# Performance work log

Hardware: AMD Instinct MI355X
Metric: run time of the kernel (lower is better)

## Reference

```python
import jax, jax.numpy as jnp
import numpy as np

B, D, T, H, E = 4, 1024, 2048, 16, 64  # batch, dim, seq_len, n_heads, hidden_dim (H*E == D)


def setup_inputs() -> dict:
    key = jax.random.key(0)
    ks = jax.random.split(key, 6)
    x = jax.random.normal(ks[0], (B, D, T), dtype=jnp.float32)            # (b, e, t) layout
    Wp = jax.random.normal(ks[1], (H, E, D), dtype=jnp.float32) / np.sqrt(D)  # per-head proj weights
    bp = jax.random.normal(ks[2], (H, E), dtype=jnp.float32) * 0.01
    tw = jax.random.normal(ks[3], (H, T), dtype=jnp.float32) / np.sqrt(T)  # per-head Toeplitz kernel, tw[h,0]=diagonal
    Wo = jax.random.normal(ks[4], (D, D), dtype=jnp.float32) / np.sqrt(D)
    bo = jax.random.normal(ks[5], (D,), dtype=jnp.float32) * 0.01
    return {"x": x, "Wp": Wp, "bp": bp, "tw": tw, "Wo": Wo, "bo": bo}


def reference(x, Wp, bp, tw, Wo, bo):
    # x: (b, dim, t) -> (b, t, dim)
    xt = jnp.transpose(x, (0, 2, 1))
    # per-head projections: (b, h, e, t)
    proj = jnp.einsum('btd,hed->bhet', xt, Wp) + bp[None, :, :, None]
    # build per-head causal lower-triangular Toeplitz matrices: Tm[h, t, s] = tw[h, t-s] if s <= t else 0
    idx = jnp.arange(T)[:, None] - jnp.arange(T)[None, :]  # (t, s)
    Tm = jnp.where(idx >= 0, tw[:, jnp.clip(idx, 0)], 0.0)  # (h, t, s)
    # causal Toeplitz mixing along time per head
    mixed = jnp.einsum('hts,bhes->bhet', Tm, proj)          # (b, h, e, t)
    # concat heads on feature dim: (b, t, h*e) == (b, t, dim)
    cat = jnp.transpose(mixed, (0, 3, 1, 2)).reshape(B, T, H * E)
    out = cat @ Wo.T + bo                                   # out_proj: Linear(dim, dim)
    return jnp.transpose(out, (0, 2, 1))                    # back to (b, e, t)
```

## Files before the change

### kernel.cpp

```cpp
#include <hip/hip_runtime.h>
#include <cstdint>

#define NB 4
#define ND 1024
#define NT 2048
#define NH 16
#define NE 64
#define GLEN 2240
#define CAP 2312

typedef __bf16 bf16x8 __attribute__((ext_vector_type(8)));
typedef float f32x4 __attribute__((ext_vector_type(4)));
typedef unsigned short us8 __attribute__((ext_vector_type(8)));
typedef unsigned short us4 __attribute__((ext_vector_type(4)));

__device__ __forceinline__ unsigned short f2bf(float f) {
  unsigned u = __builtin_bit_cast(unsigned, f);
  return (unsigned short)((u + 0x7fffu + ((u >> 16) & 1u)) >> 16);
}

__device__ __forceinline__ void gload16(const void* g, void* l) {
  __builtin_amdgcn_global_load_lds(
      (const __attribute__((address_space(1))) void*)(uintptr_t)g,
      (__attribute__((address_space(3))) void*)(uintptr_t)l, 16, 0, 0);
}

__global__ void prep_kernel(const float* __restrict__ Wp, const float* __restrict__ Wo,
                            const float* __restrict__ tw,
                            unsigned short* __restrict__ WpB, unsigned short* __restrict__ WoB,
                            unsigned short* __restrict__ Gr8) {
  int idx = blockIdx.x * 256 + threadIdx.x;
  int stride = gridDim.x * 256;
  const int n4 = ND * ND / 4;
  for (int i = idx; i < n4; i += stride) {
    float4 v = ((const float4*)Wp)[i];
    us4 o = {f2bf(v.x), f2bf(v.y), f2bf(v.z), f2bf(v.w)};
    ((us4*)WpB)[i] = o;
  }
  for (int i = idx; i < n4; i += stride) {
    float4 v = ((const float4*)Wo)[i];
    us4 o = {f2bf(v.x), f2bf(v.y), f2bf(v.z), f2bf(v.w)};
    ((us4*)WoB)[i] = o;
  }
  for (int i = idx; i < NH * 8 * GLEN; i += stride) {
    int h = i / (8 * GLEN);
    int rem = i - h * 8 * GLEN;
    int r = rem / GLEN;
    int c = rem - r * GLEN;
    int src = c + r;
    Gr8[i] = (src <= NT - 1) ? f2bf(tw[h * NT + (NT - 1) - src]) : (unsigned short)0;
  }
}

__global__ __launch_bounds__(256) void transpose_cast(const float* __restrict__ x,
                                                      unsigned short* __restrict__ xT) {
  __shared__ float tile[64][65];
  const int c = threadIdx.x & 15, r = threadIdx.x >> 4;
  const int t0 = blockIdx.x * 64, d0 = blockIdx.y * 64, b = blockIdx.z;
  const float* xb = x + (long)b * ND * NT;
#pragma unroll
  for (int k = 0; k < 4; ++k) {
    float4 v = *(const float4*)&xb[(long)(d0 + r + 16 * k) * NT + t0 + 4 * c];
    tile[r + 16 * k][4 * c + 0] = v.x;
    tile[r + 16 * k][4 * c + 1] = v.y;
    tile[r + 16 * k][4 * c + 2] = v.z;
    tile[r + 16 * k][4 * c + 3] = v.w;
  }
  __syncthreads();
  unsigned short* xTb = xT + (long)b * NT * ND;
#pragma unroll
  for (int k = 0; k < 4; ++k) {
    int t = r + 16 * k;
    us4 o = {f2bf(tile[4 * c + 0][t]), f2bf(tile[4 * c + 1][t]), f2bf(tile[4 * c + 2][t]),
             f2bf(tile[4 * c + 3][t])};
    *(us4*)&xTb[(long)(t0 + t) * ND + d0 + 4 * c] = o;
  }
}

template <bool OUT_BF16>
__global__ __launch_bounds__(512, 2) void gemm_bt(const unsigned short* __restrict__ A,
                                                  const unsigned short* __restrict__ Bt,
                                                  const float* __restrict__ bias,
                                                  void* __restrict__ Cb, long strideB,
                                                  long strideC) {
  const int N = 2048, K = 1024;
  __shared__ __align__(16) unsigned short As[3][128 * 64];
  __shared__ __align__(16) unsigned short Bs[3][256 * 64];
  const int tid = threadIdx.x;
  const int lane = tid & 63;
  const int wid = tid >> 6;
  const int wm = (wid & 1) * 64, wn = (wid >> 1) * 64;
  const int m0 = blockIdx.y * 128, n0 = blockIdx.x * 256;
  const unsigned short* Bb = Bt + (long)blockIdx.z * strideB;
  const int mlo = lane & 15, q = lane >> 4, m7 = mlo & 7;

  const int r0 = tid >> 3;
  const int xblk = (tid & 7) ^ (r0 & 7);
  const unsigned short* aSrc = A + (long)(m0 + r0) * K + xblk * 8;
  const unsigned short* bSrc = Bb + (long)(n0 + r0) * K + xblk * 8;

  auto stage0 = [&](int buf, int t) {
    gload16(aSrc + t * 64, &As[buf][tid * 8]);
    gload16(aSrc + 64 * (long)K + t * 64, &As[buf][(512 + tid) * 8]);
    gload16(bSrc + t * 64, &Bs[buf][tid * 8]);
  };
  auto stage1 = [&](int buf, int t) {
    gload16(bSrc + 64 * (long)K + t * 64, &Bs[buf][(512 + tid) * 8]);
    gload16(bSrc + 128 * (long)K + t * 64, &Bs[buf][(1024 + tid) * 8]);
    gload16(bSrc + 192 * (long)K + t * 64, &Bs[buf][(1536 + tid) * 8]);
  };

  f32x4 acc[4][4] = {};
  stage0(0, 0);
  stage1(0, 0);
  stage0(1, 1);
  stage1(1, 1);

#pragma unroll
  for (int t = 0; t < 16; ++t) {
    const int buf = t % 3;
    if (t < 15)
      asm volatile("s_waitcnt vmcnt(6) lgkmcnt(0)" ::: "memory");
    else
      asm volatile("s_waitcnt vmcnt(0) lgkmcnt(0)" ::: "memory");
    __builtin_amdgcn_s_barrier();
#pragma unroll
    for (int ks = 0; ks < 2; ++ks) {
      bf16x8 av[4], bv[4];
      const int xb8 = ((4 * ks + q) ^ m7) * 8;
#pragma unroll
      for (int i = 0; i < 4; ++i) {
        av[i] = __builtin_bit_cast(bf16x8, *(const us8*)&As[buf][(wm + i * 16 + mlo) * 64 + xb8]);
        bv[i] = __builtin_bit_cast(bf16x8, *(const us8*)&Bs[buf][(wn + i * 16 + mlo) * 64 + xb8]);
      }
      if (t + 2 < 16) {
        if (ks == 0)
          stage0((t + 2) % 3, t + 2);
        else
          stage1((t + 2) % 3, t + 2);
      }
      __builtin_amdgcn_s_setprio(1);
#pragma unroll
      for (int i = 0; i < 4; ++i)
#pragma unroll
        for (int j = 0; j < 4; ++j)
          acc[i][j] = __builtin_amdgcn_mfma_f32_16x16x32_bf16(av[i], bv[j], acc[i][j], 0, 0, 0);
      __builtin_amdgcn_s_setprio(0);
    }
  }

#pragma unroll
  for (int i = 0; i < 4; ++i)
#pragma unroll
    for (int j = 0; j < 4; ++j)
#pragma unroll
      for (int r = 0; r < 4; ++r) {
        int gr = m0 + wm + i * 16 + q * 4 + r;
        int gc = n0 + wn + j * 16 + mlo;
        float v = acc[i][j][r] + bias[gr];
        if (OUT_BF16)
          ((unsigned short*)Cb)[(long)blockIdx.z * strideC + (long)gr * N + gc] = f2bf(v);
        else
          ((float*)Cb)[(long)blockIdx.z * strideC + (long)gr * N + gc] = v;
      }
}

__global__ __launch_bounds__(256, 2) void toeplitz(const unsigned short* __restrict__ proj,
                                                   const unsigned short* __restrict__ Gr8,
                                                   unsigned short* __restrict__ mixedT) {
  __shared__ __align__(16) unsigned short Ls[8 * CAP];
  __shared__ __align__(16) unsigned short Bs[4][2][64 * 32];
  const int tid = threadIdx.x, lane = tid & 63, w = tid >> 6;
  const int j = blockIdx.x, h = blockIdx.y, bz = blockIdx.z;
  const int mlo = lane & 15, q = lane >> 4;
  const int wt = (w >> 1) * 64, we = (w & 1) * 32;
  const int t0L = (15 - j) * 128, t0S = j * 128;

  const int delta = (NT - 128) - t0L;
  const int MUSE = t0L + 256;
#pragma unroll 1
  for (int r = 0; r < 8; ++r) {
    int rr = (r + delta) & 7;
    int off8 = r + delta - rr;
    const unsigned short* src = Gr8 + (long)(h * 8 + rr) * GLEN + off8;
    unsigned short* dst = &Ls[r * CAP];
    for (int mc = tid; mc * 8 < MUSE; mc += 256) gload16(src + mc * 8, dst + mc * 8);
  }

  const int rA = (7 - mlo) & 7;
  const int eRow = tid >> 2, kCol = (tid & 3) * 8;
  const unsigned short* bsrc = proj + ((long)bz * ND + h * 64 + eRow) * NT + kCol;

  const int nc0 = 2 * (16 - j);
  const int NCT = 34;
  const unsigned short* lA0 = &Ls[rA * CAP + (127 - wt - mlo - rA) + q * 8];
  const unsigned short* lA1 = lA0 + (t0L - t0S);

  auto stage = [&](int g) {
    int c = (g < nc0) ? g : g - nc0;
    gload16(bsrc + c * 64, &Bs[g & 3][0][tid * 8]);
    gload16(bsrc + c * 64 + 32, &Bs[g & 3][1][tid * 8]);
  };

  stage(0);
  stage(1);
  stage(2);

  f32x4 acc[4][2];
  bf16x8 ap0 = {}, ap1 = {};
  const unsigned short* lA = lA0;

  auto sub = [&](int bf, int hh, int s) {
    bf16x8 a0 = __builtin_bit_cast(bf16x8, *(const us8*)(lA + s));
    bf16x8 a1 = __builtin_bit_cast(bf16x8, *(const us8*)(lA + s - 16));
    bf16x8 b0 = __builtin_bit_cast(bf16x8, *(const us8*)&Bs[bf][hh][(we + mlo) * 32 + q * 8]);
    bf16x8 b1 = __builtin_bit_cast(bf16x8, *(const us8*)&Bs[bf][hh][(we + 16 + mlo) * 32 + q * 8]);
    acc[0][0] = __builtin_amdgcn_mfma_f32_16x16x32_bf16(a0, b0, acc[0][0], 0, 0, 0);
    acc[0][1] = __builtin_amdgcn_mfma_f32_16x16x32_bf16(a0, b1, acc[0][1], 0, 0, 0);
    acc[1][0] = __builtin_amdgcn_mfma_f32_16x16x32_bf16(a1, b0, acc[1][0], 0, 0, 0);
    acc[1][1] = __builtin_amdgcn_mfma_f32_16x16x32_bf16(a1, b1, acc[1][1], 0, 0, 0);
    acc[2][0] = __builtin_amdgcn_mfma_f32_16x16x32_bf16(ap0, b0, acc[2][0], 0, 0, 0);
    acc[2][1] = __builtin_amdgcn_mfma_f32_16x16x32_bf16(ap0, b1, acc[2][1], 0, 0, 0);
    acc[3][0] = __builtin_amdgcn_mfma_f32_16x16x32_bf16(ap1, b0, acc[3][0], 0, 0, 0);
    acc[3][1] = __builtin_amdgcn_mfma_f32_16x16x32_bf16(ap1, b1, acc[3][1], 0, 0, 0);
    ap0 = a0;
    ap1 = a1;
  };

#pragma unroll 1
  for (int g = 0; g < NCT; ++g) {
    if (g + 2 < NCT)
      asm volatile("s_waitcnt vmcnt(4) lgkmcnt(0)" ::: "memory");
    else if (g + 1 < NCT)
      asm volatile("s_waitcnt vmcnt(2) lgkmcnt(0)" ::: "memory");
    else
      asm volatile("s_waitcnt vmcnt(0) lgkmcnt(0)" ::: "memory");
    __builtin_amdgcn_s_barrier();
    if (g + 3 < NCT) stage(g + 3);

    const int pass = (g >= nc0) ? 1 : 0;
    const int c = pass ? g - nc0 : g;
    if (c == 0) {
      lA = pass ? lA1 : lA0;
      ap0 = __builtin_bit_cast(bf16x8, *(const us8*)(lA - 32));
      ap1 = __builtin_bit_cast(bf16x8, *(const us8*)(lA - 48));
#pragma unroll
      for (int i = 0; i < 4; ++i)
#pragma unroll
        for (int jj = 0; jj < 2; ++jj) acc[i][jj] = f32x4{0.f, 0.f, 0.f, 0.f};
    }
    const int buf = g & 3;
    const int s0 = c * 64;
    __builtin_amdgcn_s_setprio(1);
    sub(buf, 0, s0);
    sub(buf, 1, s0 + 32);
    __builtin_amdgcn_s_setprio(0);

    if ((!pass && g == nc0 - 1) || g == NCT - 1) {
      const int t0p = pass ? t0S : t0L;
#pragma unroll
      for (int i = 0; i < 4; ++i)
#pragma unroll
        for (int jj = 0; jj < 2; ++jj)
#pragma unroll
          for (int rr = 0; rr < 4; ++rr) {
            int t = t0p + wt + i * 16 + q * 4 + rr;
            int e = we + jj * 16 + mlo;
            mixedT[((long)bz * NT + t) * ND + h * 64 + e] = f2bf(acc[i][jj][rr]);
          }
    }
  }
}

extern "C" void kernel_launch(void* const* d_in, const int* in_sizes, int n_in, void* d_out,
                              int out_size, void* d_ws, size_t ws_size, hipStream_t stream) {
  const float* x = (const float*)d_in[0];
  const float* Wp = (const float*)d_in[1];
  const float* bp = (const float*)d_in[2];
  const float* tw = (const float*)d_in[3];
  const float* Wo = (const float*)d_in[4];
  const float* bo = (const float*)d_in[5];
  float* out = (float*)d_out;

  char* ws = (char*)d_ws;
  unsigned short* xT = (unsigned short*)(ws);
  unsigned short* proj = (unsigned short*)(ws + (16ull << 20));
  unsigned short* WpB = (unsigned short*)(ws + (32ull << 20));
  unsigned short* WoB = (unsigned short*)(ws + (34ull << 20));
  unsigned short* Gr8 = (unsigned short*)(ws + (36ull << 20));

  prep_kernel<<<dim3(1024), 256, 0, stream>>>(Wp, Wo, tw, WpB, WoB, Gr8);
  transpose_cast<<<dim3(NT / 64, ND / 64, NB), 256, 0, stream>>>(x, xT);
  gemm_bt<true><<<dim3(8, 8, NB), 512, 0, stream>>>(WpB, xT, bp, proj, (long)NT * ND,
                                                    (long)ND * NT);
  toeplitz<<<dim3(8, NH, NB), 256, 0, stream>>>(proj, Gr8, xT);
  gemm_bt<false><<<dim3(8, 8, NB), 512, 0, stream>>>(WoB, xT, bo, out, (long)NT * ND,
                                                     (long)ND * NT);
}
```

Baseline: 159.7 us.

## Shrink GEMM tile to 128x128 with double buffering and swap toeplitz grid order

The projection and output GEMMs move from 512-thread blocks with 128x256 tiles and a three-stage LDS pipeline to 256-thread blocks with 128x128 tiles and two-stage double buffering. The load prefetch now happens after a barrier at the top of each iteration instead of being interleaved with the MFMA k-steps. This doubles the grid to 512 blocks for better CU occupancy on a 256-CU part, but cuts operand reuse per tile and adds an extra barrier per iteration. The toeplitz grid swaps head and chunk axes so that neighbouring blocks share the same time chunk, which may change cache locality and load balance.

```diff
diff --git a/kernel.cpp b/kernel.cpp
--- a/kernel.cpp
+++ b/kernel.cpp
@@ -78,51 +78,56 @@
 }
 
 template <bool OUT_BF16>
-__global__ __launch_bounds__(512, 2) void gemm_bt(const unsigned short* __restrict__ A,
+__global__ __launch_bounds__(256, 2) void gemm_bt(const unsigned short* __restrict__ A,
                                                   const unsigned short* __restrict__ Bt,
                                                   const float* __restrict__ bias,
                                                   void* __restrict__ Cb, long strideB,
                                                   long strideC) {
   const int N = 2048, K = 1024;
-  __shared__ __align__(16) unsigned short As[3][128 * 64];
-  __shared__ __align__(16) unsigned short Bs[3][256 * 64];
+  __shared__ __align__(16) unsigned short As[2][128 * 64];
+  __shared__ __align__(16) unsigned short Bs[2][128 * 64];
   const int tid = threadIdx.x;
   const int lane = tid & 63;
   const int wid = tid >> 6;
   const int wm = (wid & 1) * 64, wn = (wid >> 1) * 64;
-  const int m0 = blockIdx.y * 128, n0 = blockIdx.x * 256;
+  const int m0 = blockIdx.y * 128, n0 = blockIdx.x * 128;
   const unsigned short* Bb = Bt + (long)blockIdx.z * strideB;
   const int mlo = lane & 15, q = lane >> 4, m7 = mlo & 7;
 
-  const int r0 = tid >> 3;
-  const int xblk = (tid & 7) ^ (r0 & 7);
-  const unsigned short* aSrc = A + (long)(m0 + r0) * K + xblk * 8;
-  const unsigned short* bSrc = Bb + (long)(n0 + r0) * K + xblk * 8;
-
-  auto stage0 = [&](int buf, int t) {
-    gload16(aSrc + t * 64, &As[buf][tid * 8]);
-    gload16(aSrc + 64 * (long)K + t * 64, &As[buf][(512 + tid) * 8]);
-    gload16(bSrc + t * 64, &Bs[buf][tid * 8]);
+  const unsigned short* aP[4];
+  const unsigned short* bP[4];
+  int dstc[4];
+#pragma unroll
+  for (int p = 0; p < 4; ++p) {
+    int chunk = p * 256 + tid;
+    int row = chunk >> 3, blk = chunk & 7;
+    int sc = (blk ^ (row & 7)) * 8;
+    aP[p] = A + (long)(m0 + row) * K + sc;
+    bP[p] = Bb + (long)(n0 + row) * K + sc;
+    dstc[p] = chunk * 8;
+  }
+
+  auto stage = [&](int buf, int t) {
+#pragma unroll
+    for (int p = 0; p < 4; ++p) {
+      gload16(aP[p] + t * 64, &As[buf][dstc[p]]);
+      gload16(bP[p] + t * 64, &Bs[buf][dstc[p]]);
+    }
   };
-  auto stage1 = [&](int buf, int t) {
-    gload16(bSrc + 64 * (long)K + t * 64, &Bs[buf][(512 + tid) * 8]);
-    gload16(bSrc + 128 * (long)K + t * 64, &Bs[buf][(1024 + tid) * 8]);
-    gload16(bSrc + 192 * (long)K + t * 64, &Bs[buf][(1536 + tid) * 8]);
-  };
 
   f32x4 acc[4][4] = {};
-  stage0(0, 0);
-  stage1(0, 0);
-  stage0(1, 1);
-  stage1(1, 1);
+  stage(0, 0);
 
 #pragma unroll
   for (int t = 0; t < 16; ++t) {
-    const int buf = t % 3;
+    const int buf = t & 1;
+    asm volatile("s_waitcnt lgkmcnt(0)" ::: "memory");
+    __builtin_amdgcn_s_barrier();
+    if (t < 15) stage(buf ^ 1, t + 1);
     if (t < 15)
-      asm volatile("s_waitcnt vmcnt(6) lgkmcnt(0)" ::: "memory");
+      asm volatile("s_waitcnt vmcnt(8)" ::: "memory");
     else
-      asm volatile("s_waitcnt vmcnt(0) lgkmcnt(0)" ::: "memory");
+      asm volatile("s_waitcnt vmcnt(0)" ::: "memory");
     __builtin_amdgcn_s_barrier();
 #pragma unroll
     for (int ks = 0; ks < 2; ++ks) {
@@ -132,12 +137,6 @@
       for (int i = 0; i < 4; ++i) {
         av[i] = __builtin_bit_cast(bf16x8, *(const us8*)&As[buf][(wm + i * 16 + mlo) * 64 + xb8]);
         bv[i] = __builtin_bit_cast(bf16x8, *(const us8*)&Bs[buf][(wn + i * 16 + mlo) * 64 + xb8]);
-      }
-      if (t + 2 < 16) {
-        if (ks == 0)
-          stage0((t + 2) % 3, t + 2);
-        else
-          stage1((t + 2) % 3, t + 2);
       }
       __builtin_amdgcn_s_setprio(1);
 #pragma unroll
@@ -171,7 +170,7 @@
   __shared__ __align__(16) unsigned short Ls[8 * CAP];
   __shared__ __align__(16) unsigned short Bs[4][2][64 * 32];
   const int tid = threadIdx.x, lane = tid & 63, w = tid >> 6;
-  const int j = blockIdx.x, h = blockIdx.y, bz = blockIdx.z;
+  const int j = blockIdx.y, h = blockIdx.x, bz = blockIdx.z;
   const int mlo = lane & 15, q = lane >> 4;
   const int wt = (w >> 1) * 64, we = (w & 1) * 32;
   const int t0L = (15 - j) * 128, t0S = j * 128;
@@ -291,9 +290,9 @@
 
   prep_kernel<<<dim3(1024), 256, 0, stream>>>(Wp, Wo, tw, WpB, WoB, Gr8);
   transpose_cast<<<dim3(NT / 64, ND / 64, NB), 256, 0, stream>>>(x, xT);
-  gemm_bt<true><<<dim3(8, 8, NB), 512, 0, stream>>>(WpB, xT, bp, proj, (long)NT * ND,
-                                                    (long)ND * NT);
-  toeplitz<<<dim3(8, NH, NB), 256, 0, stream>>>(proj, Gr8, xT);
-  gemm_bt<false><<<dim3(8, 8, NB), 512, 0, stream>>>(WoB, xT, bo, out, (long)NT * ND,
+  gemm_bt<true><<<dim3(16, 8, NB), 256, 0, stream>>>(WpB, xT, bp, proj, (long)NT * ND,
                                                      (long)ND * NT);
-}
+  toeplitz<<<dim3(NH, 8, NB), 256, 0, stream>>>(proj, Gr8, xT);
+  gemm_bt<false><<<dim3(16, 8, NB), 256, 0, stream>>>(WoB, xT, bo, out, (long)NT * ND,
+                                                      (long)ND * NT);
+}
```

After: 155.8 us (median of 2 runs). 1.03x faster.
